# Performance work log

Hardware: AMD Instinct MI355X
Metric: run time of the kernel (lower is better)

The kernel has to match this reference:

```python
import jax, jax.numpy as jnp
import numpy as np

K = 3        # attention kernel size
PAD = 1      # padding
C = 20       # out_channels (hidden_dim_1)
HALF = C // 2
POOL = 4     # MaxPool2d((1, 4))
OUT_DIM = 80


def setup_inputs() -> dict:
    key = jax.random.key(0)
    ks = jax.random.split(key, 8)
    T, D = 1024, 1280
    lin_in = C * D // POOL  # 6400
    return {
        "feature": jax.random.normal(ks[0], (T, D), jnp.float32),
        "wq": jax.random.normal(ks[1], (C, 1), jnp.float32),
        "wk": jax.random.normal(ks[2], (C, 1), jnp.float32),
        "wv": jax.random.normal(ks[3], (C, 1), jnp.float32),
        "rel_h": jax.random.normal(ks[4], (HALF, K), jnp.float32),
        "rel_w": jax.random.normal(ks[5], (HALF, K), jnp.float32),
        "dense_w": jax.random.normal(ks[6], (OUT_DIM, lin_in), jnp.float32) * 0.02,
        "dense_b": jax.random.normal(ks[7], (OUT_DIM,), jnp.float32) * 0.02,
    }


def reference(feature, wq, wk, wv, rel_h, rel_w, dense_w, dense_b):
    T, D = feature.shape
    W = D // POOL
    # MaxPool2d((1, POOL)) over last dim of [1,1,T,D]
    x = feature.reshape(T, W, POOL).max(axis=-1)[None, None]  # [1,1,T,W]

    # 1x1 convs (in_channels=1) are just channel outer products
    q = jnp.einsum('bihw,oi->bohw', x, wq)                    # [1,C,T,W]
    xp = jnp.pad(x, ((0, 0), (0, 0), (PAD, PAD), (PAD, PAD)))
    k = jnp.einsum('bihw,oi->bohw', xp, wk)                   # [1,C,T+2,W+2]
    v = jnp.einsum('bihw,oi->bohw', xp, wv)

    # unfold(2,K,1).unfold(3,K,1) -> windows flattened as (i_h*K + i_w)
    def windows(t):
        return jnp.stack([t[:, :, i:i + T, j:j + W]
                          for i in range(K) for j in range(K)], axis=-1)  # [1,C,T,W,K*K]

    k_win = windows(k)
    v_win = windows(v)

    # relative positional bias: first HALF channels get rel_h (varies along h),
    # second HALF get rel_w (varies along w); flattened to K*K in (h,w) order
    rel = jnp.concatenate([
        jnp.broadcast_to(rel_h[:, :, None], (HALF, K, K)),
        jnp.broadcast_to(rel_w[:, None, :], (HALF, K, K)),
    ], axis=0).reshape(C, K * K)
    k_win = k_win + rel[None, :, None, None, :]

    attn = jax.nn.softmax(q[..., None] * k_win, axis=-1)      # [1,C,T,W,9]
    out = jnp.sum(attn * v_win, axis=-1)                      # [1,C,T,W]
    out = jax.nn.relu(out)

    # torch: transpose(0,1) -> [C,1,T,W] then view(-1, C*W): channel-major flatten
    flat = out[0].reshape(-1, C * W)                          # [T, C*W]
    y = flat @ dense_w.T + dense_b                            # [T, OUT_DIM]
    # torch: stack -> [T,1,OUT], transpose(0,1) -> [1,T,OUT]
    return y[None, :, :]
```

## Files before the change

### kernel.cpp

```cpp
#include <hip/hip_runtime.h>
#include <hip/hip_bf16.h>

#define TT   1024
#define DD   1280
#define WW   320
#define CC   20
#define HALF 10
#define TW   (TT*WW)
#define LIN  (CC*WW)
#define OUTD 80
#define NSPLIT 20
#define LOG2E 1.4426950408889634f
#define XPAD 384

#define POOL_BLOCKS (TW/256)
#define CVT_BLOCKS  ((OUTD*LIN)/(256*8))
#define ZERO_BLOCKS ((TT*OUTD)/(256*4))

typedef __attribute__((ext_vector_type(4))) float f32x4;
typedef __attribute__((ext_vector_type(8))) short bf16x8;

__device__ __forceinline__ ushort f2bf(float v) {
    unsigned u = __float_as_uint(v);
    u += 0x7FFFu + ((u >> 16) & 1u);
    return (ushort)(u >> 16);
}

__device__ __forceinline__ unsigned pk_bf16(float lo, float hi) {
    unsigned r;
    asm("v_cvt_pk_bf16_f32 %0, %1, %2" : "=v"(r) : "v"(lo), "v"(hi));
    return r;
}

__global__ __launch_bounds__(256) void k_prep(const float* __restrict__ f,
                                              float* __restrict__ x,
                                              const float* __restrict__ dw,
                                              ushort* __restrict__ dwb,
                                              float* __restrict__ out) {
    int b = blockIdx.x;
    if (b < POOL_BLOCKS) {
        int idx = b * 256 + threadIdx.x;
        float4 v = reinterpret_cast<const float4*>(f)[idx];
        x[idx] = fmaxf(fmaxf(v.x, v.y), fmaxf(v.z, v.w));
    } else if (b < POOL_BLOCKS + CVT_BLOCKS) {
        int q = (b - POOL_BLOCKS) * 256 + threadIdx.x;
        int r16 = q & 15;
        int kg  = (q >> 4) & 3;
        int z   = q >> 6;
        int jj  = z % 5;
        int y   = z / 5;
        int ks  = y % 10;
        int sp  = y / 10;
        const float* src = dw + (size_t)(jj * 16 + r16) * LIN + sp * 320 + ks * 32 + kg * 8;
        float4 a = reinterpret_cast<const float4*>(src)[0];
        float4 c = reinterpret_cast<const float4*>(src)[1];
        reinterpret_cast<ushort4*>(dwb + (size_t)q * 8)[0] =
            make_ushort4(f2bf(a.x), f2bf(a.y), f2bf(a.z), f2bf(a.w));
        reinterpret_cast<ushort4*>(dwb + (size_t)q * 8)[1] =
            make_ushort4(f2bf(c.x), f2bf(c.y), f2bf(c.z), f2bf(c.w));
    } else {
        int idx = (b - POOL_BLOCKS - CVT_BLOCKS) * 256 + threadIdx.x;
        reinterpret_cast<float4*>(out)[idx] = make_float4(0.f, 0.f, 0.f, 0.f);
    }
}

template<bool ISH>
__device__ __forceinline__ uint2 attn_group(const float xr[3][6], float qk,
                                            float r0, float r1, float r2, float vv) {
    float G[3][6];
    #pragma unroll
    for (int dt = 0; dt < 3; ++dt) {
        float rdt = (dt == 0) ? r0 : ((dt == 1) ? r1 : r2);
        #pragma unroll
        for (int idx = 0; idx < 6; ++idx)
            G[dt][idx] = ISH ? fmaf(qk, xr[dt][idx], rdt) : (qk * xr[dt][idx]);
    }
    float o[4];
    #pragma unroll
    for (int p = 0; p < 4; ++p) {
        float xc = xr[1][p + 1];
        float s[9];
        if (ISH) {
            #pragma unroll
            for (int i = 0; i < 9; ++i) s[i] = xc * G[i / 3][p + i % 3];
        } else {
            float bb0 = r0 * xc, bb1 = r1 * xc, bb2 = r2 * xc;
            #pragma unroll
            for (int i = 0; i < 9; ++i) {
                float bbw = ((i % 3) == 0) ? bb0 : (((i % 3) == 1) ? bb1 : bb2);
                s[i] = fmaf(xc, G[i / 3][p + i % 3], bbw);
            }
        }
        float m = fmaxf(fmaxf(fmaxf(fmaxf(s[0], s[1]), s[2]),
                              fmaxf(fmaxf(s[3], s[4]), s[5])),
                        fmaxf(fmaxf(s[6], s[7]), s[8]));
        float den0 = 0.f, den1 = 0.f, num0 = 0.f, num1 = 0.f;
        #pragma unroll
        for (int i = 0; i < 9; ++i) {
            float e = __builtin_amdgcn_exp2f(s[i] - m);
            if (i & 1) { den1 += e; num1 = fmaf(e, xr[i / 3][p + i % 3], num1); }
            else       { den0 += e; num0 = fmaf(e, xr[i / 3][p + i % 3], num0); }
        }
        float den = den0 + den1, num = num0 + num1;
        o[p] = fmaxf(vv * (num * __builtin_amdgcn_rcpf(den)), 0.0f);
    }
    return make_uint2(pk_bf16(o[0], o[1]), pk_bf16(o[2], o[3]));
}

__global__ __launch_bounds__(256, 6) void k_fused(const float* __restrict__ x,
                                                  const float* __restrict__ wq,
                                                  const float* __restrict__ wk,
                                                  const float* __restrict__ wv,
                                                  const float* __restrict__ rh,
                                                  const float* __restrict__ rw,
                                                  const ushort* __restrict__ dwb,
                                                  const float* __restrict__ bias,
                                                  float* __restrict__ out) {
    __shared__ __align__(16) ushort alds[16][328];
    __shared__ float red[2][16][81];

    int tid = threadIdx.x;
    int mt  = blockIdx.x;
    int sp  = blockIdx.y;

    {
        int j  = tid >> 4;
        int wg = tid & 15;
        int ct = (mt * 16 + j) * 20 + sp;
        int t  = ct & 1023;
        int c  = ct >> 10;
        bool ish = (c < HALF);

        float wqc = wq[c];
        float qk  = wqc * wk[c] * LOG2E;
        float vv  = wv[c];
        const float* rp = ish ? (rh + c * 3) : (rw + (c - HALF) * 3);
        float r0 = wqc * rp[0] * LOG2E;
        float r1 = wqc * rp[1] * LOG2E;
        float r2 = wqc * rp[2] * LOG2E;

        bool rok0 = (t > 0), rok2 = (t < TT - 1);
        const float* xb0 = x + t * WW;

        for (int u = 0; u < 5; ++u) {
            int gg = wg + 16 * u;
            int w0 = gg * 4;
            float xr[3][6];
            #pragma unroll
            for (int dt = 0; dt < 3; ++dt) {
                const float* rpx = xb0 + (dt - 1) * WW + w0;
                float4 va = *reinterpret_cast<const float4*>(rpx - 4);
                float4 vb = *reinterpret_cast<const float4*>(rpx);
                float  vc = rpx[4];
                bool rok = (dt == 1) ? true : ((dt == 0) ? rok0 : rok2);
                xr[dt][0] = (rok & (gg > 0))  ? va.w : 0.f;
                xr[dt][1] = rok ? vb.x : 0.f;
                xr[dt][2] = rok ? vb.y : 0.f;
                xr[dt][3] = rok ? vb.z : 0.f;
                xr[dt][4] = rok ? vb.w : 0.f;
                xr[dt][5] = (rok & (gg < 79)) ? vc : 0.f;
            }
            uint2 res = ish ? attn_group<true >(xr, qk, r0, r1, r2, vv)
                            : attn_group<false>(xr, qk, r0, r1, r2, vv);
            *reinterpret_cast<uint2*>(&alds[j][w0]) = res;
        }
    }

    __syncthreads();

    int wave = tid >> 6;
    int lane = tid & 63;
    int r16  = lane & 15;
    int kg   = lane >> 4;

    int ks0 = (wave < 2) ? wave * 3 : 6 + (wave - 2) * 2;
    int ksn = (wave < 2) ? 3 : 2;

    f32x4 acc[5] = {};
    for (int ks = ks0; ks < ks0 + ksn; ++ks) {
        bf16x8 af = *reinterpret_cast<const bf16x8*>(&alds[r16][ks * 32 + kg * 8]);
        const ushort* bp = dwb + (size_t)(((sp * 10 + ks) * 5) * 64 + lane) * 8;
        #pragma unroll
        for (int jj = 0; jj < 5; ++jj) {
            bf16x8 bfr = *reinterpret_cast<const bf16x8*>(bp + (size_t)jj * 512);
            acc[jj] = __builtin_amdgcn_mfma_f32_16x16x32_bf16(af, bfr, acc[jj], 0, 0, 0);
        }
    }

    if (wave < 2) {
        #pragma unroll
        for (int jj = 0; jj < 5; ++jj)
            #pragma unroll
            for (int r = 0; r < 4; ++r)
                red[wave][kg * 4 + r][jj * 16 + r16] = acc[jj][r];
    }
    __syncthreads();
    if (wave >= 2) {
        #pragma unroll
        for (int jj = 0; jj < 5; ++jj)
            #pragma unroll
            for (int r = 0; r < 4; ++r)
                red[wave - 2][kg * 4 + r][jj * 16 + r16] += acc[jj][r];
    }
    __syncthreads();

    float* op = out + (size_t)(mt * 16) * OUTD;
    #pragma unroll
    for (int i2 = tid; i2 < 16 * 80; i2 += 256) {
        int row = i2 / 80, col = i2 % 80;
        float v = red[0][row][col] + red[1][row][col];
        if (sp == 0) v += bias[col];
        atomicAdd(&op[i2], v);
    }
}

extern "C" void kernel_launch(void* const* d_in, const int* in_sizes, int n_in,
                              void* d_out, int out_size, void* d_ws, size_t ws_size,
                              hipStream_t stream) {
    const float* feature = (const float*)d_in[0];
    const float* wq      = (const float*)d_in[1];
    const float* wk      = (const float*)d_in[2];
    const float* wv      = (const float*)d_in[3];
    const float* rel_h   = (const float*)d_in[4];
    const float* rel_w   = (const float*)d_in[5];
    const float* dense_w = (const float*)d_in[6];
    const float* dense_b = (const float*)d_in[7];
    float* out = (float*)d_out;

    float*  ws   = (float*)d_ws;
    float*  x    = ws + XPAD;
    ushort* dwb  = (ushort*)(ws + 2 * XPAD + TW);

    k_prep <<<POOL_BLOCKS + CVT_BLOCKS + ZERO_BLOCKS, 256, 0, stream>>>(feature, x, dense_w,
                                                                        dwb, out);
    k_fused<<<dim3(TT/16, NSPLIT), 256, 0, stream>>>(x, wq, wk, wv, rel_h, rel_w,
                                                     dwb, dense_b, out);
}
```

Baseline: 28.62 us.

## Use 320-thread blocks with one output tile per wave and drop LDS reduction

```diff
diff --git a/kernel.cpp b/kernel.cpp
--- a/kernel.cpp
+++ b/kernel.cpp
@@ -65,31 +65,21 @@
 }
 
 template<bool ISH>
-__device__ __forceinline__ uint2 attn_group(const float xr[3][6], float qk,
-                                            float r0, float r1, float r2, float vv) {
-    float G[3][6];
-    #pragma unroll
-    for (int dt = 0; dt < 3; ++dt) {
-        float rdt = (dt == 0) ? r0 : ((dt == 1) ? r1 : r2);
-        #pragma unroll
-        for (int idx = 0; idx < 6; ++idx)
-            G[dt][idx] = ISH ? fmaf(qk, xr[dt][idx], rdt) : (qk * xr[dt][idx]);
-    }
+__device__ __forceinline__ uint2 attn_g(const float xr[3][6], float qk,
+                                        float r0, float r1, float r2, float vv) {
     float o[4];
     #pragma unroll
     for (int p = 0; p < 4; ++p) {
         float xc = xr[1][p + 1];
+        float a  = qk * xc;
+        float bb0 = r0 * xc, bb1 = r1 * xc, bb2 = r2 * xc;
         float s[9];
-        if (ISH) {
-            #pragma unroll
-            for (int i = 0; i < 9; ++i) s[i] = xc * G[i / 3][p + i % 3];
-        } else {
-            float bb0 = r0 * xc, bb1 = r1 * xc, bb2 = r2 * xc;
-            #pragma unroll
-            for (int i = 0; i < 9; ++i) {
-                float bbw = ((i % 3) == 0) ? bb0 : (((i % 3) == 1) ? bb1 : bb2);
-                s[i] = fmaf(xc, G[i / 3][p + i % 3], bbw);
-            }
+        #pragma unroll
+        for (int i = 0; i < 9; ++i) {
+            int dt = i / 3, dw = i % 3;
+            float bias = ISH ? ((dt == 0) ? bb0 : (dt == 1) ? bb1 : bb2)
+                             : ((dw == 0) ? bb0 : (dw == 1) ? bb1 : bb2);
+            s[i] = fmaf(a, xr[dt][p + dw], bias);
         }
         float m = fmaxf(fmaxf(fmaxf(fmaxf(s[0], s[1]), s[2]),
                               fmaxf(fmaxf(s[3], s[4]), s[5])),
@@ -107,7 +97,7 @@
     return make_uint2(pk_bf16(o[0], o[1]), pk_bf16(o[2], o[3]));
 }
 
-__global__ __launch_bounds__(256, 6) void k_fused(const float* __restrict__ x,
+__global__ __launch_bounds__(320, 8) void k_fused(const float* __restrict__ x,
                                                   const float* __restrict__ wq,
                                                   const float* __restrict__ wk,
                                                   const float* __restrict__ wv,
@@ -117,15 +107,14 @@
                                                   const float* __restrict__ bias,
                                                   float* __restrict__ out) {
     __shared__ __align__(16) ushort alds[16][328];
-    __shared__ float red[2][16][81];
 
     int tid = threadIdx.x;
     int mt  = blockIdx.x;
     int sp  = blockIdx.y;
 
     {
-        int j  = tid >> 4;
-        int wg = tid & 15;
+        int j  = tid / 20;
+        int wg = tid % 20;
         int ct = (mt * 16 + j) * 20 + sp;
         int t  = ct & 1023;
         int c  = ct >> 10;
@@ -142,8 +131,8 @@
         bool rok0 = (t > 0), rok2 = (t < TT - 1);
         const float* xb0 = x + t * WW;
 
-        for (int u = 0; u < 5; ++u) {
-            int gg = wg + 16 * u;
+        for (int u = 0; u < 4; ++u) {
+            int gg = wg + 20 * u;
             int w0 = gg * 4;
             float xr[3][6];
             #pragma unroll
@@ -160,58 +149,35 @@
                 xr[dt][4] = rok ? vb.w : 0.f;
                 xr[dt][5] = (rok & (gg < 79)) ? vc : 0.f;
             }
-            uint2 res = ish ? attn_group<true >(xr, qk, r0, r1, r2, vv)
-                            : attn_group<false>(xr, qk, r0, r1, r2, vv);
+            uint2 res = ish ? attn_g<true >(xr, qk, r0, r1, r2, vv)
+                            : attn_g<false>(xr, qk, r0, r1, r2, vv);
             *reinterpret_cast<uint2*>(&alds[j][w0]) = res;
         }
     }
 
     __syncthreads();
 
-    int wave = tid >> 6;
+    int jj   = tid >> 6;
     int lane = tid & 63;
     int r16  = lane & 15;
     int kg   = lane >> 4;
 
-    int ks0 = (wave < 2) ? wave * 3 : 6 + (wave - 2) * 2;
-    int ksn = (wave < 2) ? 3 : 2;
-
-    f32x4 acc[5] = {};
-    for (int ks = ks0; ks < ks0 + ksn; ++ks) {
-        bf16x8 af = *reinterpret_cast<const bf16x8*>(&alds[r16][ks * 32 + kg * 8]);
-        const ushort* bp = dwb + (size_t)(((sp * 10 + ks) * 5) * 64 + lane) * 8;
-        #pragma unroll
-        for (int jj = 0; jj < 5; ++jj) {
-            bf16x8 bfr = *reinterpret_cast<const bf16x8*>(bp + (size_t)jj * 512);
-            acc[jj] = __builtin_amdgcn_mfma_f32_16x16x32_bf16(af, bfr, acc[jj], 0, 0, 0);
-        }
-    }
-
-    if (wave < 2) {
-        #pragma unroll
-        for (int jj = 0; jj < 5; ++jj)
-            #pragma unroll
-            for (int r = 0; r < 4; ++r)
-                red[wave][kg * 4 + r][jj * 16 + r16] = acc[jj][r];
-    }
-    __syncthreads();
-    if (wave >= 2) {
-        #pragma unroll
-        for (int jj = 0; jj < 5; ++jj)
-            #pragma unroll
-            for (int r = 0; r < 4; ++r)
-                red[wave - 2][kg * 4 + r][jj * 16 + r16] += acc[jj][r];
-    }
-    __syncthreads();
-
-    float* op = out + (size_t)(mt * 16) * OUTD;
+    const ushort* bpb = dwb + (size_t)(((sp * 10) * 5 + jj) * 64 + lane) * 8;
+
+    f32x4 acc = {};
     #pragma unroll
-    for (int i2 = tid; i2 < 16 * 80; i2 += 256) {
-        int row = i2 / 80, col = i2 % 80;
-        float v = red[0][row][col] + red[1][row][col];
-        if (sp == 0) v += bias[col];
-        atomicAdd(&op[i2], v);
-    }
+    for (int ks = 0; ks < 10; ++ks) {
+        bf16x8 af  = *reinterpret_cast<const bf16x8*>(&alds[r16][ks * 32 + kg * 8]);
+        bf16x8 bfr = *reinterpret_cast<const bf16x8*>(bpb + (size_t)ks * 2560);
+        acc = __builtin_amdgcn_mfma_f32_16x16x32_bf16(af, bfr, acc, 0, 0, 0);
+    }
+
+    int col = jj * 16 + r16;
+    float bs = (sp == 0) ? bias[col] : 0.0f;
+    float* op = out + (size_t)(mt * 16) * OUTD + col;
+    #pragma unroll
+    for (int r = 0; r < 4; ++r)
+        atomicAdd(&op[(size_t)(kg * 4 + r) * OUTD], acc[r] + bs);
 }
 
 extern "C" void kernel_launch(void* const* d_in, const int* in_sizes, int n_in,
@@ -233,6 +199,6 @@
 
     k_prep <<<POOL_BLOCKS + CVT_BLOCKS + ZERO_BLOCKS, 256, 0, stream>>>(feature, x, dense_w,
                                                                         dwb, out);
-    k_fused<<<dim3(TT/16, NSPLIT), 256, 0, stream>>>(x, wq, wk, wv, rel_h, rel_w,
+    k_fused<<<dim3(TT/16, NSPLIT), 320, 0, stream>>>(x, wq, wk, wv, rel_h, rel_w,
                                                      dwb, dense_b, out);
 }
```

Result: slower. 29.32 us (+2.4%).
